# Optimization experiments

Hardware: AMD Instinct MI355X
Metric: run time of the kernel (lower is better)

The kernel has to match this reference:

```python
import jax, jax.numpy as jnp
import numpy as np

N = 16      # num_blocks (grid is N x N)
D = 256     # block_size (homogeneous)
B = 2048    # batch_size
ITERS = 3   # num_iterations
# Static block-sparsity: block (i, j) exists iff j <= i + 1 (banded lower grid).
MASK = np.array([[1.0 if j <= i + 1 else 0.0 for j in range(N)] for i in range(N)], dtype=np.float32)


def setup_inputs() -> dict:
    key = jax.random.key(0)
    k1, k2, k3 = jax.random.split(key, 3)
    x0 = jax.random.normal(k1, (B, D), dtype=jnp.float32)
    # W[i, j] is the (out=D, in=D) weight of the Linear mapping block j -> block i.
    W = jax.random.normal(k2, (N, N, D, D), dtype=jnp.float32) * (1.0 / np.sqrt(D))
    b = jax.random.normal(k3, (N, N, D), dtype=jnp.float32) * 0.01
    return {"x0": x0, "W": W, "b": b}


def reference(x0, W, b):
    mask = jnp.asarray(MASK)
    Wm = W * mask[:, :, None, None]   # zero out absent grid blocks
    bm = b * mask[:, :, None]
    # Iteration 1: format_input pads with None, so only input block j=0 exists;
    # row i output = blocks[i][0](x0) (bias of block (i,0) only).
    Y = jnp.einsum('bd,med->mbe', x0, Wm[:, 0]) + bm[:, 0][:, None, :]   # [N, B, D]
    Y = jax.nn.relu(Y)
    # Remaining iterations: all N block inputs are present.
    bias_full = jnp.sum(bm, axis=1)   # [N, D] sum of biases over present blocks per row
    for _ in range(ITERS - 1):
        Y = jnp.einsum('nbd,mned->mbe', Y, Wm) + bias_full[:, None, :]
        Y = jax.nn.relu(Y)
    return Y  # [N, B, D]
```

## Files before the change

kernel.cpp:

```cpp
#include <hip/hip_runtime.h>
#include <hip/hip_bf16.h>
#include <stdint.h>


#define DD    256
#define NBLK  16
#define BATCH 2048

typedef __attribute__((ext_vector_type(8))) short  bf16x8;
typedef __attribute__((ext_vector_type(8))) __bf16 bfv8;
typedef __attribute__((ext_vector_type(4))) float  f32x4;

__device__ __constant__ int Pofs[17] = {0,2,5,9,14,20,27,35,44,54,65,77,90,104,119,135,151};

__device__ __forceinline__ unsigned short f2bf(float f) {
  return __builtin_bit_cast(unsigned short, (__bf16)f);
}

__device__ __forceinline__ void gload_lds16(const unsigned short* g, unsigned short* l) {
  __builtin_amdgcn_global_load_lds((const __attribute__((address_space(1))) void*)g,
                                   (__attribute__((address_space(3))) void*)l, 16, 0, 0);
}

__device__ __forceinline__ bf16x8 cvt8(float4 lo, float4 hi) {
  bfv8 t;
  t[0] = (__bf16)lo.x; t[1] = (__bf16)lo.y; t[2] = (__bf16)lo.z; t[3] = (__bf16)lo.w;
  t[4] = (__bf16)hi.x; t[5] = (__bf16)hi.y; t[6] = (__bf16)hi.z; t[7] = (__bf16)hi.w;
  return __builtin_bit_cast(bf16x8, t);
}


__global__ void cvt_x0_kernel(const float* __restrict__ x, unsigned short* __restrict__ y) {
  int i = blockIdx.x * 256 + threadIdx.x;
  float4 v = ((const float4*)x)[i];
  ushort4 o;
  o.x = f2bf(v.x); o.y = f2bf(v.y); o.z = f2bf(v.z); o.w = f2bf(v.w);
  ((ushort4*)y)[i] = o;
}

__global__ void bias_full_kernel(const float* __restrict__ b, float* __restrict__ bf) {
  int idx = blockIdx.x * 256 + threadIdx.x;
  int m = idx >> 8, e = idx & 255;
  int nb = (m + 2 < NBLK) ? m + 2 : NBLK;
  float s = 0.f;
  for (int j = 0; j < nb; ++j) s += b[(m * NBLK + j) * DD + e];
  bf[idx] = s;
}

__global__ void cvt_W_kernel(const float* __restrict__ W, unsigned short* __restrict__ Wb) {
  int p = blockIdx.x >> 5;
  int m = 0;
#pragma unroll
  for (int k = 1; k <= 15; ++k) if (p >= Pofs[k]) m = k;
  int n = p - Pofs[m];
  long idx = (long)(blockIdx.x & 31) * 2048 + threadIdx.x * 8;
  const float* src = W + (long)(m * NBLK + n) * (DD * DD) + idx;
  float4 lo = *(const float4*)src;
  float4 hi = *(const float4*)(src + 4);
  *(bf16x8*)(Wb + (long)p * (DD * DD) + idx) = cvt8(lo, hi);
}


template <int OUT_BF16>
__global__ __launch_bounds__(256, 2) void gemm_step2(
    const unsigned short* __restrict__ A,
    const unsigned short* __restrict__ Wb,
    const float* __restrict__ bias,
    int bias_stride,
    long a_nstride,
    int nb_mode,
    void* __restrict__ Out)
{
  __shared__ unsigned short ldsA[2][128 * 64];
  __shared__ unsigned short ldsW[2][128 * 64];

  const int tid  = threadIdx.x;
  const int wave = tid >> 6;
  const int lane = tid & 63;

  int bid = blockIdx.x;
  int swz = (bid & 7) * 64 + (bid >> 3);
  int mi_ = swz >> 5;
  const int m = (int)((0x8796A5B4C3D2E1F0ULL >> (mi_ * 4)) & 15);
  int rest = swz & 31;
  const int btile = rest >> 1;
  const int etile = rest & 1;
  const int nb = nb_mode ? ((m + 2 < NBLK) ? m + 2 : NBLK) : 1;
  const int nt = nb << 2;

  const int brow0 = btile * 128;
  const int ecol0 = etile * 128;
  const int wr = (wave >> 1) & 1;
  const int wc = wave & 1;

  long a_goff[4], w_goff[4];
  int  s_lds[4];
#pragma unroll
  for (int i = 0; i < 4; ++i) {
    int inst  = wave * 4 + i;
    int row   = inst * 8 + (lane >> 3);
    int chunk = (lane & 7) ^ (row & 7);
    a_goff[i] = (long)(brow0 + row) * DD + chunk * 8;
    w_goff[i] = (long)(ecol0 + row) * DD + chunk * 8;
    s_lds[i]  = inst * 512;
  }

  int offA[4][2], offW[4][2];
#pragma unroll
  for (int f = 0; f < 4; ++f) {
    int ra = wr * 64 + f * 16 + (lane & 15);
    int rw = wc * 64 + f * 16 + (lane & 15);
#pragma unroll
    for (int ks = 0; ks < 2; ++ks) {
      int byteoff = ks * 64 + (lane >> 4) * 16;
      offA[f][ks] = ra * 64 + ((byteoff ^ ((ra & 7) << 4)) >> 1);
      offW[f][ks] = rw * 64 + ((byteoff ^ ((rw & 7) << 4)) >> 1);
    }
  }

  f32x4 acc[4][4];
#pragma unroll
  for (int i = 0; i < 4; ++i)
#pragma unroll
    for (int j = 0; j < 4; ++j) acc[i][j] = (f32x4){0.f, 0.f, 0.f, 0.f};

  const unsigned short* Wrow = Wb + (long)Pofs[m] * (DD * DD);

  auto compute = [&](int p) {
#pragma unroll
    for (int ks = 0; ks < 2; ++ks) {
      bf16x8 af[4], wf[4];
#pragma unroll
      for (int f = 0; f < 4; ++f) af[f] = *(const bf16x8*)&ldsA[p][offA[f][ks]];
#pragma unroll
      for (int f = 0; f < 4; ++f) wf[f] = *(const bf16x8*)&ldsW[p][offW[f][ks]];
#pragma unroll
      for (int i = 0; i < 4; ++i)
#pragma unroll
        for (int j = 0; j < 4; ++j)
          acc[i][j] = __builtin_amdgcn_mfma_f32_16x16x32_bf16(af[i], wf[j], acc[i][j], 0, 0, 0);
    }
  };

#pragma unroll
  for (int i = 0; i < 4; ++i) {
    gload_lds16(A + a_goff[i],    &ldsA[0][s_lds[i]]);
    gload_lds16(Wrow + w_goff[i], &ldsW[0][s_lds[i]]);
  }

  for (int t = 0; t < nt - 1; ++t) {
    const int p   = t & 1;
    const int nxt = p ^ 1;
    int n2  = (t + 1) >> 2;
    int kk2 = ((t + 1) & 3) * 64;
    const unsigned short* An = A + (long)n2 * a_nstride + kk2;
    const unsigned short* Wn = Wrow + (long)n2 * (DD * DD) + kk2;
#pragma unroll
    for (int i = 0; i < 4; ++i) {
      gload_lds16(An + a_goff[i], &ldsA[nxt][s_lds[i]]);
      gload_lds16(Wn + w_goff[i], &ldsW[nxt][s_lds[i]]);
    }
    asm volatile("s_waitcnt vmcnt(8)" ::: "memory");
    __builtin_amdgcn_s_barrier();
    compute(p);
    __builtin_amdgcn_s_barrier();
  }
  asm volatile("s_waitcnt vmcnt(0)" ::: "memory");
  __builtin_amdgcn_s_barrier();
  compute((nt - 1) & 1);

  const long outbase = (long)m * BATCH * DD;
  const int  rowbase = brow0 + wr * 64;
  const int  colbase = ecol0 + wc * 64;
  float bv[4];
#pragma unroll
  for (int j = 0; j < 4; ++j)
    bv[j] = bias[m * bias_stride + colbase + j * 16 + (lane & 15)];
#pragma unroll
  for (int i = 0; i < 4; ++i) {
#pragma unroll
    for (int r = 0; r < 4; ++r) {
      const int row = rowbase + i * 16 + ((lane >> 4) << 2) + r;
      const long rb = outbase + (long)row * DD + colbase + (lane & 15);
#pragma unroll
      for (int j = 0; j < 4; ++j) {
        float v = acc[i][j][r] + bv[j];
        v = v > 0.f ? v : 0.f;
        if (OUT_BF16) ((unsigned short*)Out)[rb + j * 16] = f2bf(v);
        else          ((float*)Out)[rb + j * 16] = v;
      }
    }
  }
}


template <int OUT_BF16>
__global__ __launch_bounds__(256, 2) void gemm_step(
    const unsigned short* __restrict__ A,
    const float* __restrict__ Wg,
    const float* __restrict__ bias,
    int bias_stride, long a_nstride, int nb_mode,
    void* __restrict__ Out)
{
  __shared__ unsigned short ldsA[2][128 * 64];
  __shared__ unsigned short ldsW[2][128 * 64];
  const int tid  = threadIdx.x;
  const int wave = tid >> 6;
  const int lane = tid & 63;
  int bid = blockIdx.x;
  int swz = (bid & 7) * 64 + (bid >> 3);
  int mi_ = swz >> 5;
  const int m = (int)((0x8796A5B4C3D2E1F0ULL >> (mi_ * 4)) & 15);
  int rest = swz & 31;
  const int btile = rest >> 1;
  const int etile = rest & 1;
  const int nb = nb_mode ? ((m + 2 < NBLK) ? m + 2 : NBLK) : 1;
  const int nt = nb << 2;
  const int brow0 = btile * 128;
  const int ecol0 = etile * 128;
  const int wr = (wave >> 1) & 1;
  const int wc = wave & 1;

  long a_goff[4]; int a_lds[4];
#pragma unroll
  for (int i = 0; i < 4; ++i) {
    int inst  = wave * 4 + i;
    int row   = inst * 8 + (lane >> 3);
    int chunk = (lane & 7) ^ (row & 7);
    a_goff[i] = (long)(brow0 + row) * DD + chunk * 8;
    a_lds[i]  = inst * 512;
  }
  long w_goff[4]; int w_lds[4];
#pragma unroll
  for (int u = 0; u < 4; ++u) {
    int cid = tid + 256 * u;
    int row = cid >> 3;
    int c16 = cid & 7;
    w_goff[u] = (long)(ecol0 + row) * DD + c16 * 8;
    w_lds[u]  = row * 64 + ((c16 ^ (row & 7)) * 8);
  }
  int offA[4][2], offW[4][2];
#pragma unroll
  for (int f = 0; f < 4; ++f) {
    int ra = wr * 64 + f * 16 + (lane & 15);
    int rw = wc * 64 + f * 16 + (lane & 15);
#pragma unroll
    for (int ks = 0; ks < 2; ++ks) {
      int byteoff = ks * 64 + (lane >> 4) * 16;
      offA[f][ks] = ra * 64 + ((byteoff ^ ((ra & 7) << 4)) >> 1);
      offW[f][ks] = rw * 64 + ((byteoff ^ ((rw & 7) << 4)) >> 1);
    }
  }
  f32x4 acc[4][4];
#pragma unroll
  for (int i = 0; i < 4; ++i)
#pragma unroll
    for (int j = 0; j < 4; ++j) acc[i][j] = (f32x4){0.f,0.f,0.f,0.f};
  const long wm_base = (long)m * NBLK * (DD * DD);
  {
#pragma unroll
    for (int i = 0; i < 4; ++i) gload_lds16(A + a_goff[i], &ldsA[0][a_lds[i]]);
    const float* Wn = Wg + wm_base;
#pragma unroll
    for (int u = 0; u < 4; ++u) {
      float4 lo = *(const float4*)(Wn + w_goff[u]);
      float4 hi = *(const float4*)(Wn + w_goff[u] + 4);
      *(bf16x8*)&ldsW[0][w_lds[u]] = cvt8(lo, hi);
    }
  }
  __syncthreads();
  int cur = 0;
  for (int t = 0; t < nt; ++t) {
    const int nxt = cur ^ 1;
    const bool has_next = (t + 1 < nt);
    float4 wlo[4], whi[4];
    if (has_next) {
      int n2  = (t + 1) >> 2;
      int kk2 = ((t + 1) & 3) * 64;
      const unsigned short* An = A + (long)n2 * a_nstride + kk2;
#pragma unroll
      for (int i = 0; i < 4; ++i) gload_lds16(An + a_goff[i], &ldsA[nxt][a_lds[i]]);
      const float* Wn = Wg + wm_base + (long)n2 * (DD * DD) + kk2;
#pragma unroll
      for (int u = 0; u < 4; ++u) {
        wlo[u] = *(const float4*)(Wn + w_goff[u]);
        whi[u] = *(const float4*)(Wn + w_goff[u] + 4);
      }
    }
#pragma unroll
    for (int ks = 0; ks < 2; ++ks) {
      bf16x8 af[4], wf[4];
#pragma unroll
      for (int f = 0; f < 4; ++f) af[f] = *(const bf16x8*)&ldsA[cur][offA[f][ks]];
#pragma unroll
      for (int f = 0; f < 4; ++f) wf[f] = *(const bf16x8*)&ldsW[cur][offW[f][ks]];
#pragma unroll
      for (int i = 0; i < 4; ++i)
#pragma unroll
        for (int j = 0; j < 4; ++j)
          acc[i][j] = __builtin_amdgcn_mfma_f32_16x16x32_bf16(af[i], wf[j], acc[i][j], 0, 0, 0);
    }
    if (has_next) {
#pragma unroll
      for (int u = 0; u < 4; ++u)
        *(bf16x8*)&ldsW[nxt][w_lds[u]] = cvt8(wlo[u], whi[u]);
    }
    __syncthreads();
    cur = nxt;
  }
  const long outbase = (long)m * BATCH * DD;
  const int  rowbase = brow0 + wr * 64;
  const int  colbase = ecol0 + wc * 64;
#pragma unroll
  for (int j = 0; j < 4; ++j) {
    const int col = colbase + j * 16 + (lane & 15);
    const float bv = bias[m * bias_stride + col];
#pragma unroll
    for (int i = 0; i < 4; ++i) {
      const int row0 = rowbase + i * 16 + ((lane >> 4) << 2);
#pragma unroll
      for (int r = 0; r < 4; ++r) {
        float v = acc[i][j][r] + bv;
        v = v > 0.f ? v : 0.f;
        long idx = outbase + (long)(row0 + r) * DD + col;
        if (OUT_BF16) ((unsigned short*)Out)[idx] = f2bf(v);
        else          ((float*)Out)[idx] = v;
      }
    }
  }
}


extern "C" void kernel_launch(void* const* d_in, const int* in_sizes, int n_in,
                              void* d_out, int out_size, void* d_ws, size_t ws_size,
                              hipStream_t stream) {
  const float* x0 = (const float*)d_in[0];
  const float* W  = (const float*)d_in[1];
  const float* b  = (const float*)d_in[2];
  float* out = (float*)d_out;

  char* ws = (char*)d_ws;
  unsigned short* x0b = (unsigned short*)ws;
  unsigned short* Y0  = (unsigned short*)(ws + (1ull << 20));
  unsigned short* Y1  = (unsigned short*)(ws + (17ull << 20));

  const size_t wb_bytes = 151ull * DD * DD * 2;
  const size_t need = (33ull << 20) + wb_bytes + 16384;

  cvt_x0_kernel<<<512, 256, 0, stream>>>(x0, x0b);

  if (ws_size >= need) {
    unsigned short* Wb = (unsigned short*)(ws + (33ull << 20));
    float* bias_full   = (float*)(ws + (33ull << 20) + wb_bytes);
    bias_full_kernel<<<16, 256, 0, stream>>>(b, bias_full);
    cvt_W_kernel<<<151 * 32, 256, 0, stream>>>(W, Wb);
    gemm_step2<1><<<512, 256, 0, stream>>>(x0b, Wb, b, NBLK * DD, 0L, 0, (void*)Y0);
    gemm_step2<1><<<512, 256, 0, stream>>>(Y0, Wb, bias_full, DD, (long)BATCH * DD, 1, (void*)Y1);
    gemm_step2<0><<<512, 256, 0, stream>>>(Y1, Wb, bias_full, DD, (long)BATCH * DD, 1, (void*)out);
  } else {
    float* bias_full = (float*)(ws + (33ull << 20));
    bias_full_kernel<<<16, 256, 0, stream>>>(b, bias_full);
    gemm_step<1><<<512, 256, 0, stream>>>(x0b, W, b, NBLK * DD, 0L, 0, (void*)Y0);
    gemm_step<1><<<512, 256, 0, stream>>>(Y0, W, bias_full, DD, (long)BATCH * DD, 1, (void*)Y1);
    gemm_step<0><<<512, 256, 0, stream>>>(Y1, W, bias_full, DD, (long)BATCH * DD, 1, (void*)out);
  }
}
```

Baseline: 254.0 us.

## Deepen GEMM LDS pipeline to four stages with 32-wide K tiles

Replaces the double-buffered 64-wide K pipeline with a four-buffer ring of 32-wide K slices. Three loads are kept in flight ahead of compute, with a prologue and drain sequence. The LDS swizzle and lane-to-chunk mapping are adjusted for the narrower tile. Total LDS use stays the same, but the loop now runs twice as many iterations, each with two barriers and less MFMA work to hide latency behind.

```diff
diff --git a/kernel.cpp b/kernel.cpp
--- a/kernel.cpp
+++ b/kernel.cpp
@@ -62,7 +62,7 @@
 
 
 template <int OUT_BF16>
-__global__ __launch_bounds__(256, 2) void gemm_step2(
+__global__ __launch_bounds__(256, 2) void gemm_step3(
     const unsigned short* __restrict__ A,
     const unsigned short* __restrict__ Wb,
     const float* __restrict__ bias,
@@ -71,8 +71,8 @@
     int nb_mode,
     void* __restrict__ Out)
 {
-  __shared__ unsigned short ldsA[2][128 * 64];
-  __shared__ unsigned short ldsW[2][128 * 64];
+  __shared__ unsigned short ldsA[4][128 * 32];
+  __shared__ unsigned short ldsW[4][128 * 32];
 
   const int tid  = threadIdx.x;
   const int wave = tid >> 6;
@@ -86,36 +86,32 @@
   const int btile = rest >> 1;
   const int etile = rest & 1;
   const int nb = nb_mode ? ((m + 2 < NBLK) ? m + 2 : NBLK) : 1;
-  const int nt = nb << 2;
+  const int nt = nb << 3;
 
   const int brow0 = btile * 128;
   const int ecol0 = etile * 128;
   const int wr = (wave >> 1) & 1;
   const int wc = wave & 1;
 
-  long a_goff[4], w_goff[4];
-  int  s_lds[4];
-#pragma unroll
-  for (int i = 0; i < 4; ++i) {
-    int inst  = wave * 4 + i;
-    int row   = inst * 8 + (lane >> 3);
-    int chunk = (lane & 7) ^ (row & 7);
+  long a_goff[2], w_goff[2];
+  int  s_lds[2];
+#pragma unroll
+  for (int i = 0; i < 2; ++i) {
+    int inst  = wave * 2 + i;
+    int row   = inst * 16 + (lane >> 2);
+    int chunk = (lane & 3) ^ (row & 3);
     a_goff[i] = (long)(brow0 + row) * DD + chunk * 8;
     w_goff[i] = (long)(ecol0 + row) * DD + chunk * 8;
     s_lds[i]  = inst * 512;
   }
 
-  int offA[4][2], offW[4][2];
+  int offA[4], offW[4];
 #pragma unroll
   for (int f = 0; f < 4; ++f) {
     int ra = wr * 64 + f * 16 + (lane & 15);
     int rw = wc * 64 + f * 16 + (lane & 15);
-#pragma unroll
-    for (int ks = 0; ks < 2; ++ks) {
-      int byteoff = ks * 64 + (lane >> 4) * 16;
-      offA[f][ks] = ra * 64 + ((byteoff ^ ((ra & 7) << 4)) >> 1);
-      offW[f][ks] = rw * 64 + ((byteoff ^ ((rw & 7) << 4)) >> 1);
-    }
+    offA[f] = ra * 32 + (((lane >> 4) ^ (ra & 3)) * 8);
+    offW[f] = rw * 32 + (((lane >> 4) ^ (rw & 3)) * 8);
   }
 
   f32x4 acc[4][4];
@@ -126,48 +122,52 @@
 
   const unsigned short* Wrow = Wb + (long)Pofs[m] * (DD * DD);
 
-  auto compute = [&](int p) {
-#pragma unroll
-    for (int ks = 0; ks < 2; ++ks) {
-      bf16x8 af[4], wf[4];
-#pragma unroll
-      for (int f = 0; f < 4; ++f) af[f] = *(const bf16x8*)&ldsA[p][offA[f][ks]];
-#pragma unroll
-      for (int f = 0; f < 4; ++f) wf[f] = *(const bf16x8*)&ldsW[p][offW[f][ks]];
-#pragma unroll
-      for (int i = 0; i < 4; ++i)
-#pragma unroll
-        for (int j = 0; j < 4; ++j)
-          acc[i][j] = __builtin_amdgcn_mfma_f32_16x16x32_bf16(af[i], wf[j], acc[i][j], 0, 0, 0);
-    }
+  auto issue = [&](int tt) {
+    int nblk = tt >> 3;
+    int kk2  = (tt & 7) * 32;
+    const unsigned short* An = A + (long)nblk * a_nstride + kk2;
+    const unsigned short* Wn = Wrow + (long)nblk * (DD * DD) + kk2;
+    int buf = tt & 3;
+    gload_lds16(An + a_goff[0], &ldsA[buf][s_lds[0]]);
+    gload_lds16(Wn + w_goff[0], &ldsW[buf][s_lds[0]]);
+    gload_lds16(An + a_goff[1], &ldsA[buf][s_lds[1]]);
+    gload_lds16(Wn + w_goff[1], &ldsW[buf][s_lds[1]]);
   };
 
-#pragma unroll
-  for (int i = 0; i < 4; ++i) {
-    gload_lds16(A + a_goff[i],    &ldsA[0][s_lds[i]]);
-    gload_lds16(Wrow + w_goff[i], &ldsW[0][s_lds[i]]);
-  }
-
-  for (int t = 0; t < nt - 1; ++t) {
-    const int p   = t & 1;
-    const int nxt = p ^ 1;
-    int n2  = (t + 1) >> 2;
-    int kk2 = ((t + 1) & 3) * 64;
-    const unsigned short* An = A + (long)n2 * a_nstride + kk2;
-    const unsigned short* Wn = Wrow + (long)n2 * (DD * DD) + kk2;
-#pragma unroll
-    for (int i = 0; i < 4; ++i) {
-      gload_lds16(An + a_goff[i], &ldsA[nxt][s_lds[i]]);
-      gload_lds16(Wn + w_goff[i], &ldsW[nxt][s_lds[i]]);
-    }
-    asm volatile("s_waitcnt vmcnt(8)" ::: "memory");
+  auto compute = [&](int tt) {
+    int buf = tt & 3;
+    bf16x8 af[4], wf[4];
+#pragma unroll
+    for (int f = 0; f < 4; ++f) af[f] = *(const bf16x8*)&ldsA[buf][offA[f]];
+#pragma unroll
+    for (int f = 0; f < 4; ++f) wf[f] = *(const bf16x8*)&ldsW[buf][offW[f]];
+#pragma unroll
+    for (int i = 0; i < 4; ++i)
+#pragma unroll
+      for (int j = 0; j < 4; ++j)
+        acc[i][j] = __builtin_amdgcn_mfma_f32_16x16x32_bf16(af[i], wf[j], acc[i][j], 0, 0, 0);
+  };
+
+  issue(0); issue(1); issue(2);
+
+  for (int t = 0; t + 3 < nt; ++t) {
+    issue(t + 3);
+    asm volatile("s_waitcnt vmcnt(12)" ::: "memory");
     __builtin_amdgcn_s_barrier();
-    compute(p);
+    compute(t);
     __builtin_amdgcn_s_barrier();
   }
+  asm volatile("s_waitcnt vmcnt(8)" ::: "memory");
+  __builtin_amdgcn_s_barrier();
+  compute(nt - 3);
+  __builtin_amdgcn_s_barrier();
+  asm volatile("s_waitcnt vmcnt(4)" ::: "memory");
+  __builtin_amdgcn_s_barrier();
+  compute(nt - 2);
+  __builtin_amdgcn_s_barrier();
   asm volatile("s_waitcnt vmcnt(0)" ::: "memory");
   __builtin_amdgcn_s_barrier();
-  compute((nt - 1) & 1);
+  compute(nt - 1);
 
   const long outbase = (long)m * BATCH * DD;
   const int  rowbase = brow0 + wr * 64;
@@ -354,9 +354,9 @@
     float* bias_full   = (float*)(ws + (33ull << 20) + wb_bytes);
     bias_full_kernel<<<16, 256, 0, stream>>>(b, bias_full);
     cvt_W_kernel<<<151 * 32, 256, 0, stream>>>(W, Wb);
-    gemm_step2<1><<<512, 256, 0, stream>>>(x0b, Wb, b, NBLK * DD, 0L, 0, (void*)Y0);
-    gemm_step2<1><<<512, 256, 0, stream>>>(Y0, Wb, bias_full, DD, (long)BATCH * DD, 1, (void*)Y1);
-    gemm_step2<0><<<512, 256, 0, stream>>>(Y1, Wb, bias_full, DD, (long)BATCH * DD, 1, (void*)out);
+    gemm_step3<1><<<512, 256, 0, stream>>>(x0b, Wb, b, NBLK * DD, 0L, 0, (void*)Y0);
+    gemm_step3<1><<<512, 256, 0, stream>>>(Y0, Wb, bias_full, DD, (long)BATCH * DD, 1, (void*)Y1);
+    gemm_step3<0><<<512, 256, 0, stream>>>(Y1, Wb, bias_full, DD, (long)BATCH * DD, 1, (void*)out);
   } else {
     float* bias_full = (float*)(ws + (33ull << 20));
     bias_full_kernel<<<16, 256, 0, stream>>>(b, bias_full);
```

After: 279.4 us. 10.0% more time.

## Load weight fragments directly from global into registers, bypassing LDS

Applied to the files above, without the earlier changes.

Weight tiles are no longer staged through LDS. Each lane now reads its bf16 MFMA B-operand fragments straight from global memory (relying on L2/cache reuse), and only the activation tile stays double-buffered in LDS. This halves LDS footprint and LDS traffic and reduces the vmcnt wait depth. The trade-off is that weight loads are now synchronous register loads inside the compute step and are not prefetched, so their global latency can stall the MFMAs. Weight data is also re-read by both wave rows.

```diff
diff --git a/kernel.cpp b/kernel.cpp
--- a/kernel.cpp
+++ b/kernel.cpp
@@ -62,7 +62,7 @@
 
 
 template <int OUT_BF16>
-__global__ __launch_bounds__(256, 2) void gemm_step2(
+__global__ __launch_bounds__(256, 2) void gemm_step4(
     const unsigned short* __restrict__ A,
     const unsigned short* __restrict__ Wb,
     const float* __restrict__ bias,
@@ -72,7 +72,6 @@
     void* __restrict__ Out)
 {
   __shared__ unsigned short ldsA[2][128 * 64];
-  __shared__ unsigned short ldsW[2][128 * 64];
 
   const int tid  = threadIdx.x;
   const int wave = tid >> 6;
@@ -93,7 +92,7 @@
   const int wr = (wave >> 1) & 1;
   const int wc = wave & 1;
 
-  long a_goff[4], w_goff[4];
+  long a_goff[4];
   int  s_lds[4];
 #pragma unroll
   for (int i = 0; i < 4; ++i) {
@@ -101,20 +100,17 @@
     int row   = inst * 8 + (lane >> 3);
     int chunk = (lane & 7) ^ (row & 7);
     a_goff[i] = (long)(brow0 + row) * DD + chunk * 8;
-    w_goff[i] = (long)(ecol0 + row) * DD + chunk * 8;
     s_lds[i]  = inst * 512;
   }
 
-  int offA[4][2], offW[4][2];
+  int offA[4][2];
 #pragma unroll
   for (int f = 0; f < 4; ++f) {
     int ra = wr * 64 + f * 16 + (lane & 15);
-    int rw = wc * 64 + f * 16 + (lane & 15);
 #pragma unroll
     for (int ks = 0; ks < 2; ++ks) {
       int byteoff = ks * 64 + (lane >> 4) * 16;
       offA[f][ks] = ra * 64 + ((byteoff ^ ((ra & 7) << 4)) >> 1);
-      offW[f][ks] = rw * 64 + ((byteoff ^ ((rw & 7) << 4)) >> 1);
     }
   }
 
@@ -125,49 +121,51 @@
     for (int j = 0; j < 4; ++j) acc[i][j] = (f32x4){0.f, 0.f, 0.f, 0.f};
 
   const unsigned short* Wrow = Wb + (long)Pofs[m] * (DD * DD);
-
-  auto compute = [&](int p) {
+  const unsigned short* Wlane =
+      Wrow + (long)(ecol0 + wc * 64 + (lane & 15)) * DD + ((lane >> 4) << 3);
+
+  auto compute = [&](int t) {
+    const int p = t & 1;
+    const unsigned short* Wt = Wlane + (long)(t >> 2) * (DD * DD) + (t & 3) * 64;
+    bf16x8 wf[2][4];
+#pragma unroll
+    for (int ks = 0; ks < 2; ++ks)
+#pragma unroll
+      for (int f = 0; f < 4; ++f)
+        wf[ks][f] = *(const bf16x8*)(Wt + f * 16 * DD + ks * 32);
 #pragma unroll
     for (int ks = 0; ks < 2; ++ks) {
-      bf16x8 af[4], wf[4];
+      bf16x8 af[4];
 #pragma unroll
       for (int f = 0; f < 4; ++f) af[f] = *(const bf16x8*)&ldsA[p][offA[f][ks]];
 #pragma unroll
-      for (int f = 0; f < 4; ++f) wf[f] = *(const bf16x8*)&ldsW[p][offW[f][ks]];
-#pragma unroll
       for (int i = 0; i < 4; ++i)
 #pragma unroll
         for (int j = 0; j < 4; ++j)
-          acc[i][j] = __builtin_amdgcn_mfma_f32_16x16x32_bf16(af[i], wf[j], acc[i][j], 0, 0, 0);
+          acc[i][j] = __builtin_amdgcn_mfma_f32_16x16x32_bf16(af[i], wf[ks][j], acc[i][j], 0, 0, 0);
     }
   };
 
 #pragma unroll
-  for (int i = 0; i < 4; ++i) {
-    gload_lds16(A + a_goff[i],    &ldsA[0][s_lds[i]]);
-    gload_lds16(Wrow + w_goff[i], &ldsW[0][s_lds[i]]);
-  }
+  for (int i = 0; i < 4; ++i)
+    gload_lds16(A + a_goff[i], &ldsA[0][s_lds[i]]);
 
   for (int t = 0; t < nt - 1; ++t) {
-    const int p   = t & 1;
-    const int nxt = p ^ 1;
     int n2  = (t + 1) >> 2;
     int kk2 = ((t + 1) & 3) * 64;
     const unsigned short* An = A + (long)n2 * a_nstride + kk2;
-    const unsigned short* Wn = Wrow + (long)n2 * (DD * DD) + kk2;
-#pragma unroll
-    for (int i = 0; i < 4; ++i) {
+    const int nxt = (t + 1) & 1;
+#pragma unroll
+    for (int i = 0; i < 4; ++i)
       gload_lds16(An + a_goff[i], &ldsA[nxt][s_lds[i]]);
-      gload_lds16(Wn + w_goff[i], &ldsW[nxt][s_lds[i]]);
-    }
-    asm volatile("s_waitcnt vmcnt(8)" ::: "memory");
+    asm volatile("s_waitcnt vmcnt(4)" ::: "memory");
     __builtin_amdgcn_s_barrier();
-    compute(p);
+    compute(t);
     __builtin_amdgcn_s_barrier();
   }
   asm volatile("s_waitcnt vmcnt(0)" ::: "memory");
   __builtin_amdgcn_s_barrier();
-  compute((nt - 1) & 1);
+  compute(nt - 1);
 
   const long outbase = (long)m * BATCH * DD;
   const int  rowbase = brow0 + wr * 64;
@@ -354,9 +352,9 @@
     float* bias_full   = (float*)(ws + (33ull << 20) + wb_bytes);
     bias_full_kernel<<<16, 256, 0, stream>>>(b, bias_full);
     cvt_W_kernel<<<151 * 32, 256, 0, stream>>>(W, Wb);
-    gemm_step2<1><<<512, 256, 0, stream>>>(x0b, Wb, b, NBLK * DD, 0L, 0, (void*)Y0);
-    gemm_step2<1><<<512, 256, 0, stream>>>(Y0, Wb, bias_full, DD, (long)BATCH * DD, 1, (void*)Y1);
-    gemm_step2<0><<<512, 256, 0, stream>>>(Y1, Wb, bias_full, DD, (long)BATCH * DD, 1, (void*)out);
+    gemm_step4<1><<<512, 256, 0, stream>>>(x0b, Wb, b, NBLK * DD, 0L, 0, (void*)Y0);
+    gemm_step4<1><<<512, 256, 0, stream>>>(Y0, Wb, bias_full, DD, (long)BATCH * DD, 1, (void*)Y1);
+    gemm_step4<0><<<512, 256, 0, stream>>>(Y1, Wb, bias_full, DD, (long)BATCH * DD, 1, (void*)out);
   } else {
     float* bias_full = (float*)(ws + (33ull << 20));
     bias_full_kernel<<<16, 256, 0, stream>>>(b, bias_full);
```

New measurement: 347.9 us. +37.0%, slower.

## Split long GEMM rows into balanced K-partitions with partial-sum combine kernel

Applied to the files above, without the earlier changes.

For iterations two and three, the triangular block rows, whose reduction lengths vary, are split into 25 work units of roughly equal K-length (at most 8 blocks), launched as 800 workgroups instead of 512. Rows 7-15 are split into two K halves whose fp32 partials go to a workspace buffer, and a combine kernel adds them with bias and ReLU. This targets the load imbalance and tail effect of the uneven per-row work. In exchange it adds two extra launches and extra fp32 partial traffic. The fallback path that read fp32 W directly is removed.

```diff
diff --git a/kernel.cpp b/kernel.cpp
--- a/kernel.cpp
+++ b/kernel.cpp
@@ -6,12 +6,20 @@
 #define DD    256
 #define NBLK  16
 #define BATCH 2048
+#define BD    (BATCH * DD)
 
 typedef __attribute__((ext_vector_type(8))) short  bf16x8;
 typedef __attribute__((ext_vector_type(8))) __bf16 bfv8;
 typedef __attribute__((ext_vector_type(4))) float  f32x4;
 
 __device__ __constant__ int Pofs[17] = {0,2,5,9,14,20,27,35,44,54,65,77,90,104,119,135,151};
+
+__device__ __constant__ int unit_tbl[25][4] = {
+  {6,0,8,-1},{0,0,2,-1},{13,0,8,12},{1,0,3,-1},{14,0,8,14},{2,0,4,-1},{14,8,8,15},
+  {7,5,4,1},{15,0,8,16},{3,0,5,-1},{15,8,8,17},{7,0,5,0},{5,0,7,-1},{8,0,5,2},
+  {11,0,7,8},{8,5,5,3},{12,0,7,10},{9,6,5,5},{12,7,7,11},{4,0,6,-1},{13,8,7,13},
+  {9,0,6,4},{10,0,6,6},{10,6,6,7},{11,7,6,9}
+};
 
 __device__ __forceinline__ unsigned short f2bf(float f) {
   return __builtin_bit_cast(unsigned short, (__bf16)f);
@@ -61,14 +69,192 @@
 }
 
 
+template <int OUT_BF16, int TAG>
+__global__ __launch_bounds__(256, 2) void gemm_unit(
+    const unsigned short* __restrict__ A,
+    const unsigned short* __restrict__ Wb,
+    const float* __restrict__ bias_full,
+    float* __restrict__ P,
+    void* __restrict__ Out)
+{
+  __shared__ unsigned short ldsA[2][128 * 64];
+  __shared__ unsigned short ldsW[2][128 * 64];
+
+  const int tid  = threadIdx.x;
+  const int wave = tid >> 6;
+  const int lane = tid & 63;
+
+  int bid = blockIdx.x;
+  int swz = (bid & 7) * 100 + (bid >> 3);
+  const int u     = swz >> 5;
+  const int tile  = swz & 31;
+  const int m    = unit_tbl[u][0];
+  const int n0   = unit_tbl[u][1];
+  const int nn   = unit_tbl[u][2];
+  const int slot = unit_tbl[u][3];
+  const int nt   = nn << 2;
+
+  const int btile = tile >> 1;
+  const int etile = tile & 1;
+  const int brow0 = btile * 128;
+  const int ecol0 = etile * 128;
+  const int wr = (wave >> 1) & 1;
+  const int wc = wave & 1;
+
+  long a_goff[4], w_goff[4];
+  int  s_lds[4];
+#pragma unroll
+  for (int i = 0; i < 4; ++i) {
+    int inst  = wave * 4 + i;
+    int row   = inst * 8 + (lane >> 3);
+    int chunk = (lane & 7) ^ (row & 7);
+    a_goff[i] = (long)(brow0 + row) * DD + chunk * 8;
+    w_goff[i] = (long)(ecol0 + row) * DD + chunk * 8;
+    s_lds[i]  = inst * 512;
+  }
+
+  int offA[4][2], offW[4][2];
+#pragma unroll
+  for (int f = 0; f < 4; ++f) {
+    int ra = wr * 64 + f * 16 + (lane & 15);
+    int rw = wc * 64 + f * 16 + (lane & 15);
+#pragma unroll
+    for (int ks = 0; ks < 2; ++ks) {
+      int byteoff = ks * 64 + (lane >> 4) * 16;
+      offA[f][ks] = ra * 64 + ((byteoff ^ ((ra & 7) << 4)) >> 1);
+      offW[f][ks] = rw * 64 + ((byteoff ^ ((rw & 7) << 4)) >> 1);
+    }
+  }
+
+  f32x4 acc[4][4];
+#pragma unroll
+  for (int i = 0; i < 4; ++i)
+#pragma unroll
+    for (int j = 0; j < 4; ++j) acc[i][j] = (f32x4){0.f, 0.f, 0.f, 0.f};
+
+  const unsigned short* Wrow = Wb + (long)(Pofs[m] + n0) * (DD * DD);
+  const unsigned short* A0   = A + (long)n0 * BD;
+
+  auto compute = [&](int p) {
+#pragma unroll
+    for (int ks = 0; ks < 2; ++ks) {
+      bf16x8 af[4], wf[4];
+#pragma unroll
+      for (int f = 0; f < 4; ++f) af[f] = *(const bf16x8*)&ldsA[p][offA[f][ks]];
+#pragma unroll
+      for (int f = 0; f < 4; ++f) wf[f] = *(const bf16x8*)&ldsW[p][offW[f][ks]];
+#pragma unroll
+      for (int i = 0; i < 4; ++i)
+#pragma unroll
+        for (int j = 0; j < 4; ++j)
+          acc[i][j] = __builtin_amdgcn_mfma_f32_16x16x32_bf16(af[i], wf[j], acc[i][j], 0, 0, 0);
+    }
+  };
+
+#pragma unroll
+  for (int i = 0; i < 4; ++i) {
+    gload_lds16(A0 + a_goff[i],   &ldsA[0][s_lds[i]]);
+    gload_lds16(Wrow + w_goff[i], &ldsW[0][s_lds[i]]);
+  }
+
+  for (int t = 0; t < nt - 1; ++t) {
+    const int p   = t & 1;
+    const int nxt = p ^ 1;
+    int n2  = (t + 1) >> 2;
+    int kk2 = ((t + 1) & 3) * 64;
+    const unsigned short* An = A0 + (long)n2 * BD + kk2;
+    const unsigned short* Wn = Wrow + (long)n2 * (DD * DD) + kk2;
+#pragma unroll
+    for (int i = 0; i < 4; ++i) {
+      gload_lds16(An + a_goff[i], &ldsA[nxt][s_lds[i]]);
+      gload_lds16(Wn + w_goff[i], &ldsW[nxt][s_lds[i]]);
+    }
+    asm volatile("s_waitcnt vmcnt(8)" ::: "memory");
+    __builtin_amdgcn_s_barrier();
+    compute(p);
+    __builtin_amdgcn_s_barrier();
+  }
+  asm volatile("s_waitcnt vmcnt(0)" ::: "memory");
+  __builtin_amdgcn_s_barrier();
+  compute((nt - 1) & 1);
+
+  const int rowbase = brow0 + wr * 64;
+  const int colbase = ecol0 + wc * 64;
+  if (slot >= 0) {
+    float* Pd = P + (long)slot * BD;
+#pragma unroll
+    for (int i = 0; i < 4; ++i) {
+#pragma unroll
+      for (int r = 0; r < 4; ++r) {
+        const int row = rowbase + i * 16 + ((lane >> 4) << 2) + r;
+        const long rb = (long)row * DD + colbase + (lane & 15);
+#pragma unroll
+        for (int j = 0; j < 4; ++j) Pd[rb + j * 16] = acc[i][j][r];
+      }
+    }
+  } else {
+    const long outbase = (long)m * BD;
+    float bv[4];
+#pragma unroll
+    for (int j = 0; j < 4; ++j)
+      bv[j] = bias_full[m * DD + colbase + j * 16 + (lane & 15)];
+#pragma unroll
+    for (int i = 0; i < 4; ++i) {
+#pragma unroll
+      for (int r = 0; r < 4; ++r) {
+        const int row = rowbase + i * 16 + ((lane >> 4) << 2) + r;
+        const long rb = outbase + (long)row * DD + colbase + (lane & 15);
+#pragma unroll
+        for (int j = 0; j < 4; ++j) {
+          float v = acc[i][j][r] + bv[j];
+          v = v > 0.f ? v : 0.f;
+          if (OUT_BF16) ((unsigned short*)Out)[rb + j * 16] = f2bf(v);
+          else          ((float*)Out)[rb + j * 16] = v;
+        }
+      }
+    }
+  }
+}
+
 template <int OUT_BF16>
+__global__ void combine_kernel(const float* __restrict__ P,
+                               const float* __restrict__ bias_full,
+                               void* __restrict__ Out) {
+  int gid = blockIdx.x;
+  int mi  = gid >> 8;
+  int m   = mi + 7;
+  long i0 = ((long)(gid & 255) * 256 + threadIdx.x) * 8;
+  const float* P0 = P + (long)(2 * mi) * BD + i0;
+  const float* P1 = P0 + BD;
+  int col = (int)(i0 & 255);
+  float4 a0 = *(const float4*)P0, a1 = *(const float4*)(P0 + 4);
+  float4 b0 = *(const float4*)P1, b1 = *(const float4*)(P1 + 4);
+  float4 c0 = *(const float4*)(bias_full + m * DD + col);
+  float4 c1 = *(const float4*)(bias_full + m * DD + col + 4);
+  float v[8] = {a0.x+b0.x+c0.x, a0.y+b0.y+c0.y, a0.z+b0.z+c0.z, a0.w+b0.w+c0.w,
+                a1.x+b1.x+c1.x, a1.y+b1.y+c1.y, a1.z+b1.z+c1.z, a1.w+b1.w+c1.w};
+#pragma unroll
+  for (int k = 0; k < 8; ++k) v[k] = v[k] > 0.f ? v[k] : 0.f;
+  long o = (long)m * BD + i0;
+  if (OUT_BF16) {
+    bfv8 t;
+#pragma unroll
+    for (int k = 0; k < 8; ++k) t[k] = (__bf16)v[k];
+    *(bf16x8*)((unsigned short*)Out + o) = __builtin_bit_cast(bf16x8, t);
+  } else {
+    float* op = (float*)Out + o;
+    *(float4*)op       = (float4){v[0], v[1], v[2], v[3]};
+    *(float4*)(op + 4) = (float4){v[4], v[5], v[6], v[7]};
+  }
+}
+
+
+template <int OUT_BF16, int TAG>
 __global__ __launch_bounds__(256, 2) void gemm_step2(
     const unsigned short* __restrict__ A,
     const unsigned short* __restrict__ Wb,
     const float* __restrict__ bias,
-    int bias_stride,
-    long a_nstride,
-    int nb_mode,
+    int bias_stride, long a_nstride, int nb_mode,
     void* __restrict__ Out)
 {
   __shared__ unsigned short ldsA[2][128 * 64];
@@ -169,7 +355,7 @@
   __builtin_amdgcn_s_barrier();
   compute((nt - 1) & 1);
 
-  const long outbase = (long)m * BATCH * DD;
+  const long outbase = (long)m * BD;
   const int  rowbase = brow0 + wr * 64;
   const int  colbase = ecol0 + wc * 64;
   float bv[4];
@@ -188,143 +374,6 @@
         v = v > 0.f ? v : 0.f;
         if (OUT_BF16) ((unsigned short*)Out)[rb + j * 16] = f2bf(v);
         else          ((float*)Out)[rb + j * 16] = v;
-      }
-    }
-  }
-}
-
-
-template <int OUT_BF16>
-__global__ __launch_bounds__(256, 2) void gemm_step(
-    const unsigned short* __restrict__ A,
-    const float* __restrict__ Wg,
-    const float* __restrict__ bias,
-    int bias_stride, long a_nstride, int nb_mode,
-    void* __restrict__ Out)
-{
-  __shared__ unsigned short ldsA[2][128 * 64];
-  __shared__ unsigned short ldsW[2][128 * 64];
-  const int tid  = threadIdx.x;
-  const int wave = tid >> 6;
-  const int lane = tid & 63;
-  int bid = blockIdx.x;
-  int swz = (bid & 7) * 64 + (bid >> 3);
-  int mi_ = swz >> 5;
-  const int m = (int)((0x8796A5B4C3D2E1F0ULL >> (mi_ * 4)) & 15);
-  int rest = swz & 31;
-  const int btile = rest >> 1;
-  const int etile = rest & 1;
-  const int nb = nb_mode ? ((m + 2 < NBLK) ? m + 2 : NBLK) : 1;
-  const int nt = nb << 2;
-  const int brow0 = btile * 128;
-  const int ecol0 = etile * 128;
-  const int wr = (wave >> 1) & 1;
-  const int wc = wave & 1;
-
-  long a_goff[4]; int a_lds[4];
-#pragma unroll
-  for (int i = 0; i < 4; ++i) {
-    int inst  = wave * 4 + i;
-    int row   = inst * 8 + (lane >> 3);
-    int chunk = (lane & 7) ^ (row & 7);
-    a_goff[i] = (long)(brow0 + row) * DD + chunk * 8;
-    a_lds[i]  = inst * 512;
-  }
-  long w_goff[4]; int w_lds[4];
-#pragma unroll
-  for (int u = 0; u < 4; ++u) {
-    int cid = tid + 256 * u;
-    int row = cid >> 3;
-    int c16 = cid & 7;
-    w_goff[u] = (long)(ecol0 + row) * DD + c16 * 8;
-    w_lds[u]  = row * 64 + ((c16 ^ (row & 7)) * 8);
-  }
-  int offA[4][2], offW[4][2];
-#pragma unroll
-  for (int f = 0; f < 4; ++f) {
-    int ra = wr * 64 + f * 16 + (lane & 15);
-    int rw = wc * 64 + f * 16 + (lane & 15);
-#pragma unroll
-    for (int ks = 0; ks < 2; ++ks) {
-      int byteoff = ks * 64 + (lane >> 4) * 16;
-      offA[f][ks] = ra * 64 + ((byteoff ^ ((ra & 7) << 4)) >> 1);
-      offW[f][ks] = rw * 64 + ((byteoff ^ ((rw & 7) << 4)) >> 1);
-    }
-  }
-  f32x4 acc[4][4];
-#pragma unroll
-  for (int i = 0; i < 4; ++i)
-#pragma unroll
-    for (int j = 0; j < 4; ++j) acc[i][j] = (f32x4){0.f,0.f,0.f,0.f};
-  const long wm_base = (long)m * NBLK * (DD * DD);
-  {
-#pragma unroll
-    for (int i = 0; i < 4; ++i) gload_lds16(A + a_goff[i], &ldsA[0][a_lds[i]]);
-    const float* Wn = Wg + wm_base;
-#pragma unroll
-    for (int u = 0; u < 4; ++u) {
-      float4 lo = *(const float4*)(Wn + w_goff[u]);
-      float4 hi = *(const float4*)(Wn + w_goff[u] + 4);
-      *(bf16x8*)&ldsW[0][w_lds[u]] = cvt8(lo, hi);
-    }
-  }
-  __syncthreads();
-  int cur = 0;
-  for (int t = 0; t < nt; ++t) {
-    const int nxt = cur ^ 1;
-    const bool has_next = (t + 1 < nt);
-    float4 wlo[4], whi[4];
-    if (has_next) {
-      int n2  = (t + 1) >> 2;
-      int kk2 = ((t + 1) & 3) * 64;
-      const unsigned short* An = A + (long)n2 * a_nstride + kk2;
-#pragma unroll
-      for (int i = 0; i < 4; ++i) gload_lds16(An + a_goff[i], &ldsA[nxt][a_lds[i]]);
-      const float* Wn = Wg + wm_base + (long)n2 * (DD * DD) + kk2;
-#pragma unroll
-      for (int u = 0; u < 4; ++u) {
-        wlo[u] = *(const float4*)(Wn + w_goff[u]);
-        whi[u] = *(const float4*)(Wn + w_goff[u] + 4);
-      }
-    }
-#pragma unroll
-    for (int ks = 0; ks < 2; ++ks) {
-      bf16x8 af[4], wf[4];
-#pragma unroll
-      for (int f = 0; f < 4; ++f) af[f] = *(const bf16x8*)&ldsA[cur][offA[f][ks]];
-#pragma unroll
-      for (int f = 0; f < 4; ++f) wf[f] = *(const bf16x8*)&ldsW[cur][offW[f][ks]];
-#pragma unroll
-      for (int i = 0; i < 4; ++i)
-#pragma unroll
-        for (int j = 0; j < 4; ++j)
-          acc[i][j] = __builtin_amdgcn_mfma_f32_16x16x32_bf16(af[i], wf[j], acc[i][j], 0, 0, 0);
-    }
-    if (has_next) {
-#pragma unroll
-      for (int u = 0; u < 4; ++u)
-        *(bf16x8*)&ldsW[nxt][w_lds[u]] = cvt8(wlo[u], whi[u]);
-    }
-    __syncthreads();
-    cur = nxt;
-  }
-  const long outbase = (long)m * BATCH * DD;
-  const int  rowbase = brow0 + wr * 64;
-  const int  colbase = ecol0 + wc * 64;
-#pragma unroll
-  for (int j = 0; j < 4; ++j) {
-    const int col = colbase + j * 16 + (lane & 15);
-    const float bv = bias[m * bias_stride + col];
-#pragma unroll
-    for (int i = 0; i < 4; ++i) {
-      const int row0 = rowbase + i * 16 + ((lane >> 4) << 2);
-#pragma unroll
-      for (int r = 0; r < 4; ++r) {
-        float v = acc[i][j][r] + bv;
-        v = v > 0.f ? v : 0.f;
-        long idx = outbase + (long)(row0 + r) * DD + col;
-        if (OUT_BF16) ((unsigned short*)Out)[idx] = f2bf(v);
-        else          ((float*)Out)[idx] = v;
       }
     }
   }
@@ -343,25 +392,26 @@
   unsigned short* x0b = (unsigned short*)ws;
   unsigned short* Y0  = (unsigned short*)(ws + (1ull << 20));
   unsigned short* Y1  = (unsigned short*)(ws + (17ull << 20));
-
-  const size_t wb_bytes = 151ull * DD * DD * 2;
-  const size_t need = (33ull << 20) + wb_bytes + 16384;
+  unsigned short* Wb  = (unsigned short*)(ws + (33ull << 20));
+  float* bias_full    = (float*)(ws + (52ull << 20));
+  float* Part         = (float*)(ws + (53ull << 20));
+
+  const size_t need_v4    = (52ull << 20) + 16384;
+  const size_t need_split = (53ull << 20) + 18ull * BD * 4;
 
   cvt_x0_kernel<<<512, 256, 0, stream>>>(x0, x0b);
-
-  if (ws_size >= need) {
-    unsigned short* Wb = (unsigned short*)(ws + (33ull << 20));
-    float* bias_full   = (float*)(ws + (33ull << 20) + wb_bytes);
-    bias_full_kernel<<<16, 256, 0, stream>>>(b, bias_full);
-    cvt_W_kernel<<<151 * 32, 256, 0, stream>>>(W, Wb);
-    gemm_step2<1><<<512, 256, 0, stream>>>(x0b, Wb, b, NBLK * DD, 0L, 0, (void*)Y0);
-    gemm_step2<1><<<512, 256, 0, stream>>>(Y0, Wb, bias_full, DD, (long)BATCH * DD, 1, (void*)Y1);
-    gemm_step2<0><<<512, 256, 0, stream>>>(Y1, Wb, bias_full, DD, (long)BATCH * DD, 1, (void*)out);
-  } else {
-    float* bias_full = (float*)(ws + (33ull << 20));
-    bias_full_kernel<<<16, 256, 0, stream>>>(b, bias_full);
-    gemm_step<1><<<512, 256, 0, stream>>>(x0b, W, b, NBLK * DD, 0L, 0, (void*)Y0);
-    gemm_step<1><<<512, 256, 0, stream>>>(Y0, W, bias_full, DD, (long)BATCH * DD, 1, (void*)Y1);
-    gemm_step<0><<<512, 256, 0, stream>>>(Y1, W, bias_full, DD, (long)BATCH * DD, 1, (void*)out);
-  }
-}
+  bias_full_kernel<<<16, 256, 0, stream>>>(b, bias_full);
+  cvt_W_kernel<<<151 * 32, 256, 0, stream>>>(W, Wb);
+
+  gemm_step2<1, 1><<<512, 256, 0, stream>>>(x0b, Wb, b, NBLK * DD, 0L, 0, (void*)Y0);
+
+  if (ws_size >= need_split) {
+    gemm_unit<1, 2><<<800, 256, 0, stream>>>(Y0, Wb, bias_full, Part, (void*)Y1);
+    combine_kernel<1><<<9 * 256, 256, 0, stream>>>(Part, bias_full, (void*)Y1);
+    gemm_unit<0, 3><<<800, 256, 0, stream>>>(Y1, Wb, bias_full, Part, (void*)out);
+    combine_kernel<0><<<9 * 256, 256, 0, stream>>>(Part, bias_full, (void*)out);
+  } else if (ws_size >= need_v4) {
+    gemm_step2<1, 2><<<512, 256, 0, stream>>>(Y0, Wb, bias_full, DD, (long)BD, 1, (void*)Y1);
+    gemm_step2<0, 3><<<512, 256, 0, stream>>>(Y1, Wb, bias_full, DD, (long)BD, 1, (void*)out);
+  }
+}
```

Result: slower. 268.1 us (+5.6%).
